# Kernel optimization log

Measured on AMD Instinct MI355X. Metric: run time of the kernel, lower is better.

## Reference

```python
import jax, jax.numpy as jnp
import numpy as np

EMBED_DIM = 1280
NUM_HEADS = 20
HEAD_DIM = EMBED_DIM // NUM_HEADS
SEQ = 1024
BSZ = 8
ROPE_BASE = 10000.0


def _rope_cos_sin(seq_len, dim, dtype):
    # ESM RotaryEmbedding: inv_freq over even indices, emb = concat(freqs, freqs)
    inv_freq = 1.0 / (ROPE_BASE ** (jnp.arange(0, dim, 2, dtype=jnp.float32) / dim))
    t = jnp.arange(seq_len, dtype=jnp.float32)
    freqs = t[:, None] * inv_freq[None, :]          # [S, D/2]
    emb = jnp.concatenate([freqs, freqs], axis=-1)  # [S, D]
    return jnp.cos(emb).astype(dtype), jnp.sin(emb).astype(dtype)


def _rotate_half(x):
    x1, x2 = jnp.split(x, 2, axis=-1)
    return jnp.concatenate([-x2, x1], axis=-1)


def _apply_rotary(x, cos, sin):
    # x: [B, H, S, D]; cos/sin: [S, D] broadcast over B, H
    return x * cos[None, None, :, :] + _rotate_half(x) * sin[None, None, :, :]


def setup_inputs() -> dict:
    key = jax.random.key(0)
    ks = jax.random.split(key, 9)
    s = 0.02
    return {
        "query": jax.random.normal(ks[0], (SEQ, BSZ, EMBED_DIM), jnp.float32),
        "q_w": jax.random.normal(ks[1], (EMBED_DIM, EMBED_DIM), jnp.float32) * s,
        "q_b": jax.random.normal(ks[2], (EMBED_DIM,), jnp.float32) * s,
        "k_w": jax.random.normal(ks[3], (EMBED_DIM, EMBED_DIM), jnp.float32) * s,
        "k_b": jax.random.normal(ks[4], (EMBED_DIM,), jnp.float32) * s,
        "v_w": jax.random.normal(ks[5], (EMBED_DIM, EMBED_DIM), jnp.float32) * s,
        "v_b": jax.random.normal(ks[6], (EMBED_DIM,), jnp.float32) * s,
        "out_w": jax.random.normal(ks[7], (EMBED_DIM, EMBED_DIM), jnp.float32) * s,
        "out_b": jax.random.normal(ks[8], (EMBED_DIM,), jnp.float32) * s,
    }


def reference(query, q_w, q_b, k_w, k_b, v_w, v_b, out_w, out_b):
    T, B, E = query.shape
    H, D = NUM_HEADS, HEAD_DIM
    scaling = D ** -0.5

    # Separate Q/K/V projections (self-attention: key = value = query)
    q = query @ q_w.T + q_b
    k = query @ k_w.T + k_b
    v = query @ v_w.T + v_b

    # [T, B, E] -> [B, H, T, D]
    def split_heads(x):
        return x.reshape(T, B, H, D).transpose(1, 2, 0, 3)

    q, k, v = split_heads(q), split_heads(k), split_heads(v)

    # Rotary embeddings on q, k
    cos, sin = _rope_cos_sin(T, D, q.dtype)
    q = _apply_rotary(q, cos, sin)
    k = _apply_rotary(k, cos, sin)

    # SDPA with explicit scale = head_dim^-0.5
    scores = jnp.einsum("bhtd,bhsd->bhts", q, k) * scaling
    probs = jax.nn.softmax(scores, axis=-1)
    attn = jnp.einsum("bhts,bhsd->bhtd", probs, v)  # [B, H, T, D]

    # [B, H, T, D] -> [T, B, E]
    attn = attn.transpose(2, 0, 1, 3).reshape(T, B, E)
    return attn @ out_w.T + out_b
```

## Files before the change

### kernel.cpp

```cpp
#include <hip/hip_runtime.h>
#include <math.h>

#define T_SEQ 1024
#define BSZ   8
#define EMB   1280
#define NH    20
#define HD    64
#define MROWS 8192
#define KBYTES (EMB * 2)

typedef __attribute__((ext_vector_type(8))) short bf16x8;
typedef __attribute__((ext_vector_type(4))) float f32x4;

__device__ __forceinline__ short f2bf(float f) {
    unsigned u = __float_as_uint(f);
    u += 0x7fff + ((u >> 16) & 1);
    return (short)(u >> 16);
}
__device__ __forceinline__ float bf2f(short s) {
    return __uint_as_float(((unsigned)(unsigned short)s) << 16);
}

__device__ __forceinline__ void gld16(const void* g, void* l) {
    __builtin_amdgcn_global_load_lds(
        (const __attribute__((address_space(1))) void*)g,
        (__attribute__((address_space(3))) void*)l, 16, 0, 0);
}

__global__ __launch_bounds__(256) void f2bf_kernel(
    const float* __restrict__ in, short* __restrict__ out, int n8)
{
    int i = blockIdx.x * 256 + threadIdx.x;
    if (i >= n8) return;
    const float4* p = (const float4*)in;
    float4 x = p[2 * i], y = p[2 * i + 1];
    bf16x8 o;
    o[0] = f2bf(x.x); o[1] = f2bf(x.y); o[2] = f2bf(x.z); o[3] = f2bf(x.w);
    o[4] = f2bf(y.x); o[5] = f2bf(y.y); o[6] = f2bf(y.z); o[7] = f2bf(y.w);
    ((bf16x8*)out)[i] = o;
}

__global__ __launch_bounds__(256) void wcast_kernel(
    const float* __restrict__ w0, const float* __restrict__ w1,
    const float* __restrict__ w2, const float* __restrict__ w3,
    short* __restrict__ o0, short* __restrict__ o1,
    short* __restrict__ o2, short* __restrict__ o3, int n8)
{
    int which = blockIdx.y;
    const float* in = (which == 0) ? w0 : (which == 1) ? w1 : (which == 2) ? w2 : w3;
    short* out      = (which == 0) ? o0 : (which == 1) ? o1 : (which == 2) ? o2 : o3;
    int i = blockIdx.x * 256 + threadIdx.x;
    if (i >= n8) return;
    const float4* p = (const float4*)in;
    float4 x = p[2 * i], y = p[2 * i + 1];
    bf16x8 o;
    o[0] = f2bf(x.x); o[1] = f2bf(x.y); o[2] = f2bf(x.z); o[3] = f2bf(x.w);
    o[4] = f2bf(y.x); o[5] = f2bf(y.y); o[6] = f2bf(y.z); o[7] = f2bf(y.w);
    ((bf16x8*)out)[i] = o;
}

__global__ void rope_table_kernel(float* __restrict__ cost, float* __restrict__ sint) {
    int idx = blockIdx.x * 256 + threadIdx.x;
    if (idx >= T_SEQ * 32) return;
    int i = idx & 31, t = idx >> 5;
    float inv = powf(10000.0f, -(float)i / 32.0f);
    float f = (float)t * inv;
    cost[idx] = cosf(f);
    sint[idx] = sinf(f);
}

__device__ __forceinline__ void gemm_core(
    const short* __restrict__ A, const short* __restrict__ B,
    char* As, char* Bs, int m0, int n0, int tid, f32x4 (&acc)[4][4])
{
    const int l   = tid & 63;
    const int wid = tid >> 6;
    const int wr  = wid >> 1, wc = wid & 1;

    const int srow = l >> 3;
    const int scol = ((l & 7) ^ srow) << 4;
    const int g16  = (l >> 4) << 4;
    const int swx  = (l & 7) << 4;

    for (int k0 = 0; k0 < EMB; k0 += 64) {
        __syncthreads();
        #pragma unroll
        for (int c = 0; c < 4; ++c) {
            int ch  = wid * 4 + c;
            int row = ch * 8 + srow;
            gld16((const char*)A + (size_t)(m0 + row) * KBYTES + k0 * 2 + scol,
                  As + ch * 1024);
            gld16((const char*)B + (size_t)(n0 + row) * KBYTES + k0 * 2 + scol,
                  Bs + ch * 1024);
        }
        __syncthreads();
        #pragma unroll
        for (int kk = 0; kk < 2; ++kk) {
            const int cb = (kk * 64 + g16) ^ swx;
            bf16x8 af[4], bfr[4];
            #pragma unroll
            for (int m = 0; m < 4; ++m)
                af[m] = *(const bf16x8*)(As + (wr * 64 + m * 16 + (l & 15)) * 128 + cb);
            #pragma unroll
            for (int n = 0; n < 4; ++n)
                bfr[n] = *(const bf16x8*)(Bs + (wc * 64 + n * 16 + (l & 15)) * 128 + cb);
            #pragma unroll
            for (int m = 0; m < 4; ++m)
                #pragma unroll
                for (int n = 0; n < 4; ++n)
                    acc[m][n] = __builtin_amdgcn_mfma_f32_16x16x32_bf16(
                        af[m], bfr[n], acc[m][n], 0, 0, 0);
        }
    }
}

__global__ __launch_bounds__(256) void qkv_gemm_kernel(
    const short* __restrict__ A,
    const short* __restrict__ B0, const short* __restrict__ B1, const short* __restrict__ B2,
    const float* __restrict__ bias0, const float* __restrict__ bias1, const float* __restrict__ bias2,
    const float* __restrict__ cost, const float* __restrict__ sint,
    short* __restrict__ O0, short* __restrict__ O1, short* __restrict__ O2)
{
    __shared__ short As_s[8192];
    __shared__ short Bs_s[8192];

    const int z = blockIdx.z;
    const short* B = (z == 0) ? B0 : (z == 1) ? B1 : B2;
    const float* bias = (z == 0) ? bias0 : (z == 1) ? bias1 : bias2;
    short* O = (z == 0) ? O0 : (z == 1) ? O1 : O2;
    const float scale = (z == 0) ? 0.125f : 1.0f;

    const int tid = threadIdx.x;
    const int l = tid & 63;
    const int wid = tid >> 6;
    const int wr = wid >> 1, wc = wid & 1;
    const int m0 = blockIdx.x * 128;
    const int n0 = blockIdx.y * 128;

    f32x4 acc[4][4];
    const f32x4 z4 = {0.f, 0.f, 0.f, 0.f};
    #pragma unroll
    for (int m = 0; m < 4; ++m)
        #pragma unroll
        for (int n = 0; n < 4; ++n) acc[m][n] = z4;

    gemm_core(A, B, (char*)As_s, (char*)Bs_s, m0, n0, tid, acc);

    #pragma unroll
    for (int n = 0; n < 4; ++n) {
        int col = n0 + wc * 64 + n * 16 + (l & 15);
        float bv = bias[col];
        #pragma unroll
        for (int m = 0; m < 4; ++m)
            #pragma unroll
            for (int r = 0; r < 4; ++r) acc[m][n][r] += bv;
    }

    if (z < 2) {
        #pragma unroll
        for (int m = 0; m < 4; ++m) {
            #pragma unroll
            for (int r = 0; r < 4; ++r) {
                int row = m0 + wr * 64 + m * 16 + (l >> 4) * 4 + r;
                int t = row >> 3;
                #pragma unroll
                for (int n = 0; n < 2; ++n) {
                    int i = n * 16 + (l & 15);
                    float c = cost[t * 32 + i];
                    float s = sint[t * 32 + i];
                    float x1 = acc[m][n][r], x2 = acc[m][n + 2][r];
                    acc[m][n][r]     = x1 * c - x2 * s;
                    acc[m][n + 2][r] = x2 * c + x1 * s;
                }
            }
        }
    }

    #pragma unroll
    for (int n = 0; n < 4; ++n) {
        int col = n0 + wc * 64 + n * 16 + (l & 15);
        int h = col >> 6, d = col & 63;
        #pragma unroll
        for (int m = 0; m < 4; ++m) {
            #pragma unroll
            for (int r = 0; r < 4; ++r) {
                int row = m0 + wr * 64 + m * 16 + (l >> 4) * 4 + r;
                int t = row >> 3, b = row & 7;
                O[((size_t)(b * NH + h) * T_SEQ + t) * HD + d] = f2bf(acc[m][n][r] * scale);
            }
        }
    }
}

__global__ __launch_bounds__(256) void out_gemm_kernel(
    const short* __restrict__ A, const short* __restrict__ B,
    const float* __restrict__ bias, float* __restrict__ O)
{
    __shared__ short As_s[8192];
    __shared__ short Bs_s[8192];

    const int tid = threadIdx.x;
    const int l = tid & 63;
    const int wid = tid >> 6;
    const int wr = wid >> 1, wc = wid & 1;
    const int m0 = blockIdx.x * 128;
    const int n0 = blockIdx.y * 128;

    f32x4 acc[4][4];
    const f32x4 z4 = {0.f, 0.f, 0.f, 0.f};
    #pragma unroll
    for (int m = 0; m < 4; ++m)
        #pragma unroll
        for (int n = 0; n < 4; ++n) acc[m][n] = z4;

    gemm_core(A, B, (char*)As_s, (char*)Bs_s, m0, n0, tid, acc);

    #pragma unroll
    for (int n = 0; n < 4; ++n) {
        int col = n0 + wc * 64 + n * 16 + (l & 15);
        float bv = bias[col];
        #pragma unroll
        for (int m = 0; m < 4; ++m) {
            #pragma unroll
            for (int r = 0; r < 4; ++r) {
                int row = m0 + wr * 64 + m * 16 + (l >> 4) * 4 + r;
                O[(size_t)row * EMB + col] = acc[m][n][r] + bv;
            }
        }
    }
}

__global__ __launch_bounds__(256) void transpose_v_kernel(
    const short* __restrict__ v, short* __restrict__ vt)
{
    __shared__ short tv[64][72];
    const int tid = threadIdx.x;
    const int bh = blockIdx.y, t0 = blockIdx.x * 64;
    const short* src = v + ((size_t)bh * T_SEQ + t0) * HD;
    #pragma unroll
    for (int p = 0; p < 2; ++p) {
        int row = p * 32 + (tid >> 3);
        int c8 = (tid & 7) * 8;
        *(bf16x8*)&tv[row][c8] = *(const bf16x8*)(src + row * HD + c8);
    }
    __syncthreads();
    short* dst = vt + (size_t)bh * (HD * T_SEQ) + t0;
    #pragma unroll
    for (int p = 0; p < 2; ++p) {
        int d = p * 32 + (tid >> 3);
        int t8 = (tid & 7) * 8;
        bf16x8 o;
        #pragma unroll
        for (int j = 0; j < 8; ++j) o[j] = tv[t8 + j][d];
        *(bf16x8*)(dst + (size_t)d * T_SEQ + t8) = o;
    }
}

__global__ __launch_bounds__(256) void attn_kernel(
    const short* __restrict__ Q, const short* __restrict__ K,
    const short* __restrict__ Vt, short* __restrict__ Aout)
{
    __shared__ short Ks_s[8192];
    __shared__ short Vs_s[8192];
    __shared__ short Ps_s[4096];
    char* Ks = (char*)Ks_s;
    char* Vs = (char*)Vs_s;
    char* Ps = (char*)Ps_s;

    const int tid = threadIdx.x;
    const int l = tid & 63;
    const int w = tid >> 6;
    const int g = l >> 4;

    const int bid = blockIdx.y * 16 + blockIdx.x;
    const int swz = (bid & 7) * 320 + (bid >> 3);
    const int q0 = (swz & 15) * 64;
    const int bh = swz >> 4;

    const int srow = l >> 3;
    const int scol = ((l & 7) ^ srow) << 4;
    const int g16  = g << 4;
    const int swx  = (l & 7) << 4;

    const short* Qg = Q + (size_t)bh * (T_SEQ * HD);
    const short* Kg = K + (size_t)bh * (T_SEQ * HD);
    const short* Vg = Vt + (size_t)bh * (HD * T_SEQ);

    #pragma unroll
    for (int c = 0; c < 2; ++c) {
        int ch = w * 2 + c;
        int row = ch * 8 + srow;
        gld16((const char*)Qg + (size_t)(q0 + row) * HD * 2 + scol, Ps + ch * 1024);
        gld16((const char*)Kg + (size_t)(row) * HD * 2 + scol, Ks + ch * 1024);
        gld16((const char*)Vg + ((size_t)row * T_SEQ) * 2 + scol, Vs + ch * 1024);
    }
    __syncthreads();

    bf16x8 qf[2];
    #pragma unroll
    for (int kk = 0; kk < 2; ++kk)
        qf[kk] = *(const bf16x8*)(Ps + (w * 16 + (l & 15)) * 128 + ((kk * 64 + g16) ^ swx));

    f32x4 oacc[4];
    const f32x4 z4 = {0.f, 0.f, 0.f, 0.f};
    #pragma unroll
    for (int n = 0; n < 4; ++n) oacc[n] = z4;
    float m_i = -INFINITY;
    float l_i = 0.f;

    const int pbase = (w * 16 + (l & 15)) * 128;

    int buf = 0;
    for (int kt = 0; kt < T_SEQ / 64; ++kt) {
        if (kt + 1 < T_SEQ / 64) {
            const int ob = (buf ^ 1) * 8192;
            #pragma unroll
            for (int c = 0; c < 2; ++c) {
                int ch = w * 2 + c;
                int row = ch * 8 + srow;
                gld16((const char*)Kg + (size_t)((kt + 1) * 64 + row) * HD * 2 + scol,
                      Ks + ob + ch * 1024);
                gld16((const char*)Vg + ((size_t)row * T_SEQ + (kt + 1) * 64) * 2 + scol,
                      Vs + ob + ch * 1024);
            }
        }
        const int cbuf = buf * 8192;

        f32x4 sT[4];
        #pragma unroll
        for (int n = 0; n < 4; ++n) sT[n] = z4;
        __builtin_amdgcn_s_setprio(1);
        #pragma unroll
        for (int kk = 0; kk < 2; ++kk) {
            const int cb = (kk * 64 + g16) ^ swx;
            #pragma unroll
            for (int n = 0; n < 4; ++n) {
                bf16x8 kf = *(const bf16x8*)(Ks + cbuf + (n * 16 + (l & 15)) * 128 + cb);
                sT[n] = __builtin_amdgcn_mfma_f32_16x16x32_bf16(kf, qf[kk], sT[n], 0, 0, 0);
            }
        }
        __builtin_amdgcn_s_setprio(0);

        float pmax = fmaxf(fmaxf(sT[0][0], sT[0][1]), fmaxf(sT[0][2], sT[0][3]));
        #pragma unroll
        for (int n = 1; n < 4; ++n)
            pmax = fmaxf(pmax, fmaxf(fmaxf(sT[n][0], sT[n][1]), fmaxf(sT[n][2], sT[n][3])));
        pmax = fmaxf(pmax, __shfl_xor(pmax, 16));
        pmax = fmaxf(pmax, __shfl_xor(pmax, 32));

        if (__any(pmax > m_i + 8.0f)) {
            float mn = fmaxf(m_i, pmax);
            float corr = __expf(m_i - mn);
            m_i = mn;
            l_i *= corr;
            #pragma unroll
            for (int r = 0; r < 4; ++r) {
                float cp = __shfl(corr, (l & 48) | (g * 4 + r));
                #pragma unroll
                for (int n = 0; n < 4; ++n) oacc[n][r] *= cp;
            }
        }

        float lsum = 0.f;
        #pragma unroll
        for (int n = 0; n < 4; ++n) {
            float p0 = __expf(sT[n][0] - m_i);
            float p1 = __expf(sT[n][1] - m_i);
            float p2 = __expf(sT[n][2] - m_i);
            float p3 = __expf(sT[n][3] - m_i);
            lsum += (p0 + p1) + (p2 + p3);
            unsigned lo = ((unsigned)(unsigned short)f2bf(p0)) |
                          (((unsigned)(unsigned short)f2bf(p1)) << 16);
            unsigned hi = ((unsigned)(unsigned short)f2bf(p2)) |
                          (((unsigned)(unsigned short)f2bf(p3)) << 16);
            uint2 pk; pk.x = lo; pk.y = hi;
            *(uint2*)(Ps + pbase + ((n * 32 + g * 8) ^ swx)) = pk;
        }
        lsum += __shfl_xor(lsum, 16);
        lsum += __shfl_xor(lsum, 32);
        l_i += lsum;

        __builtin_amdgcn_s_setprio(1);
        #pragma unroll
        for (int kk = 0; kk < 2; ++kk) {
            const int cb = (kk * 64 + g16) ^ swx;
            bf16x8 ap = *(const bf16x8*)(Ps + pbase + cb);
            #pragma unroll
            for (int n = 0; n < 4; ++n) {
                bf16x8 bv = *(const bf16x8*)(Vs + cbuf + (n * 16 + (l & 15)) * 128 + cb);
                oacc[n] = __builtin_amdgcn_mfma_f32_16x16x32_bf16(ap, bv, oacc[n], 0, 0, 0);
            }
        }
        __builtin_amdgcn_s_setprio(0);

        __syncthreads();
        buf ^= 1;
    }

    float inv = 1.0f / l_i;
    float invp[4];
    #pragma unroll
    for (int r = 0; r < 4; ++r) invp[r] = __shfl(inv, (l & 48) | (g * 4 + r));

    const int b_ = bh / NH, h = bh % NH;
    #pragma unroll
    for (int n = 0; n < 4; ++n) {
        int d = h * HD + n * 16 + (l & 15);
        #pragma unroll
        for (int r = 0; r < 4; ++r) {
            int t = q0 + w * 16 + g * 4 + r;
            Aout[((size_t)t * BSZ + b_) * EMB + d] = f2bf(oacc[n][r] * invp[r]);
        }
    }
}

extern "C" void kernel_launch(void* const* d_in, const int* in_sizes, int n_in,
                              void* d_out, int out_size, void* d_ws, size_t ws_size,
                              hipStream_t stream) {
    const float* X     = (const float*)d_in[0];
    const float* q_w   = (const float*)d_in[1];
    const float* q_b   = (const float*)d_in[2];
    const float* k_w   = (const float*)d_in[3];
    const float* k_b   = (const float*)d_in[4];
    const float* v_w   = (const float*)d_in[5];
    const float* v_b   = (const float*)d_in[6];
    const float* out_w = (const float*)d_in[7];
    const float* out_b = (const float*)d_in[8];
    float* out = (float*)d_out;

    short* ws = (short*)d_ws;
    const size_t NACT = (size_t)MROWS * EMB;
    const size_t NW   = (size_t)EMB * EMB;
    short* xb  = ws;
    short* wqb = xb + NACT;
    short* wkb = wqb + NW;
    short* wvb = wkb + NW;
    short* wob = wvb + NW;
    short* qb  = wob + NW;
    short* kb  = qb + NACT;
    short* vb  = kb + NACT;
    short* vtb = vb + NACT;
    short* ab  = vtb + NACT;
    float* cost = (float*)(ab + NACT);
    float* sint = cost + T_SEQ * 32;

    rope_table_kernel<<<dim3(128), 256, 0, stream>>>(cost, sint);
    f2bf_kernel<<<dim3(5120), 256, 0, stream>>>(X, xb, (int)(NACT / 8));
    wcast_kernel<<<dim3(800, 4), 256, 0, stream>>>(
        q_w, k_w, v_w, out_w, wqb, wkb, wvb, wob, (int)(NW / 8));

    qkv_gemm_kernel<<<dim3(MROWS / 128, EMB / 128, 3), 256, 0, stream>>>(
        xb, wqb, wkb, wvb, q_b, k_b, v_b, cost, sint, qb, kb, vb);

    transpose_v_kernel<<<dim3(T_SEQ / 64, BSZ * NH), 256, 0, stream>>>(vb, vtb);

    attn_kernel<<<dim3(T_SEQ / 64, BSZ * NH), 256, 0, stream>>>(qb, kb, vtb, ab);

    out_gemm_kernel<<<dim3(MROWS / 128, EMB / 128), 256, 0, stream>>>(
        ab, wob, out_b, out);
}
```

Measured before the change: 377.6 us.

## Double-buffer LDS with 512-thread 256x128 GEMM tiles and async prefetch

Rewrites the shared GEMM core to use two LDS buffers, prefetching k-tile t+2 with global_load_lds while computing tile t, using explicit vmcnt waits and barriers. Block size grows to 512 threads (8 waves) covering a 256x128 output tile, and setprio raises MFMA priority. The aim is to hide global-load latency and halve B-tile reloads per output row. In exchange, LDS use rises to 96KB per block, which lowers occupancy, and the grid for each GEMM gets smaller.

```diff
diff --git a/kernel.cpp b/kernel.cpp
--- a/kernel.cpp
+++ b/kernel.cpp
@@ -8,6 +8,7 @@
 #define HD    64
 #define MROWS 8192
 #define KBYTES (EMB * 2)
+#define NKT   20
 
 typedef __attribute__((ext_vector_type(8))) short bf16x8;
 typedef __attribute__((ext_vector_type(4))) float f32x4;
@@ -69,31 +70,50 @@
     sint[idx] = sinf(f);
 }
 
-__device__ __forceinline__ void gemm_core(
+__device__ __forceinline__ void gemm_stage(
     const short* __restrict__ A, const short* __restrict__ B,
-    char* As, char* Bs, int m0, int n0, int tid, f32x4 (&acc)[4][4])
+    char* As, char* Bs, int m0, int n0, int k0, int w, int srow, int scol)
+{
+    #pragma unroll
+    for (int c = 0; c < 4; ++c) {
+        int ch = w * 4 + c;
+        int row = ch * 8 + srow;
+        gld16((const char*)A + (size_t)(m0 + row) * KBYTES + k0 * 2 + scol,
+              As + ch * 1024);
+    }
+    #pragma unroll
+    for (int c = 0; c < 2; ++c) {
+        int ch = w * 2 + c;
+        int row = ch * 8 + srow;
+        gld16((const char*)B + (size_t)(n0 + row) * KBYTES + k0 * 2 + scol,
+              Bs + ch * 1024);
+    }
+}
+
+__device__ __forceinline__ void gemm_core512(
+    const short* __restrict__ A, const short* __restrict__ B,
+    char* As0, char* Bs0, char* As1, char* Bs1,
+    int m0, int n0, int tid, f32x4 (&acc)[4][4])
 {
     const int l   = tid & 63;
-    const int wid = tid >> 6;
-    const int wr  = wid >> 1, wc = wid & 1;
+    const int w   = tid >> 6;
+    const int wr  = w >> 1, wc = w & 1;
 
     const int srow = l >> 3;
     const int scol = ((l & 7) ^ srow) << 4;
     const int g16  = (l >> 4) << 4;
     const int swx  = (l & 7) << 4;
 
-    for (int k0 = 0; k0 < EMB; k0 += 64) {
-        __syncthreads();
-        #pragma unroll
-        for (int c = 0; c < 4; ++c) {
-            int ch  = wid * 4 + c;
-            int row = ch * 8 + srow;
-            gld16((const char*)A + (size_t)(m0 + row) * KBYTES + k0 * 2 + scol,
-                  As + ch * 1024);
-            gld16((const char*)B + (size_t)(n0 + row) * KBYTES + k0 * 2 + scol,
-                  Bs + ch * 1024);
-        }
-        __syncthreads();
+    gemm_stage(A, B, As0, Bs0, m0, n0, 0,  w, srow, scol);
+    gemm_stage(A, B, As1, Bs1, m0, n0, 64, w, srow, scol);
+    asm volatile("s_waitcnt vmcnt(6)" ::: "memory");
+    __builtin_amdgcn_s_barrier();
+    asm volatile("" ::: "memory");
+
+    for (int t = 0; t < NKT; ++t) {
+        char* As = (t & 1) ? As1 : As0;
+        char* Bs = (t & 1) ? Bs1 : Bs0;
+
         #pragma unroll
         for (int kk = 0; kk < 2; ++kk) {
             const int cb = (kk * 64 + g16) ^ swx;
@@ -104,25 +124,41 @@
             #pragma unroll
             for (int n = 0; n < 4; ++n)
                 bfr[n] = *(const bf16x8*)(Bs + (wc * 64 + n * 16 + (l & 15)) * 128 + cb);
+            __builtin_amdgcn_s_setprio(1);
             #pragma unroll
             for (int m = 0; m < 4; ++m)
                 #pragma unroll
                 for (int n = 0; n < 4; ++n)
                     acc[m][n] = __builtin_amdgcn_mfma_f32_16x16x32_bf16(
                         af[m], bfr[n], acc[m][n], 0, 0, 0);
-        }
-    }
-}
-
-__global__ __launch_bounds__(256) void qkv_gemm_kernel(
+            __builtin_amdgcn_s_setprio(0);
+        }
+
+        asm volatile("" ::: "memory");
+        __builtin_amdgcn_s_barrier();
+        asm volatile("" ::: "memory");
+
+        if (t + 2 < NKT)
+            gemm_stage(A, B, As, Bs, m0, n0, (t + 2) * 64, w, srow, scol);
+
+        if (t + 2 < NKT) { asm volatile("s_waitcnt vmcnt(6)" ::: "memory"); }
+        else             { asm volatile("s_waitcnt vmcnt(0)" ::: "memory"); }
+        __builtin_amdgcn_s_barrier();
+        asm volatile("" ::: "memory");
+    }
+}
+
+__global__ __launch_bounds__(512) void qkv_gemm_kernel(
     const short* __restrict__ A,
     const short* __restrict__ B0, const short* __restrict__ B1, const short* __restrict__ B2,
     const float* __restrict__ bias0, const float* __restrict__ bias1, const float* __restrict__ bias2,
     const float* __restrict__ cost, const float* __restrict__ sint,
     short* __restrict__ O0, short* __restrict__ O1, short* __restrict__ O2)
 {
-    __shared__ short As_s[8192];
-    __shared__ short Bs_s[8192];
+    __shared__ short As0_s[16384];
+    __shared__ short Bs0_s[8192];
+    __shared__ short As1_s[16384];
+    __shared__ short Bs1_s[8192];
 
     const int z = blockIdx.z;
     const short* B = (z == 0) ? B0 : (z == 1) ? B1 : B2;
@@ -134,7 +170,7 @@
     const int l = tid & 63;
     const int wid = tid >> 6;
     const int wr = wid >> 1, wc = wid & 1;
-    const int m0 = blockIdx.x * 128;
+    const int m0 = blockIdx.x * 256;
     const int n0 = blockIdx.y * 128;
 
     f32x4 acc[4][4];
@@ -144,7 +180,8 @@
         #pragma unroll
         for (int n = 0; n < 4; ++n) acc[m][n] = z4;
 
-    gemm_core(A, B, (char*)As_s, (char*)Bs_s, m0, n0, tid, acc);
+    gemm_core512(A, B, (char*)As0_s, (char*)Bs0_s, (char*)As1_s, (char*)Bs1_s,
+                 m0, n0, tid, acc);
 
     #pragma unroll
     for (int n = 0; n < 4; ++n) {
@@ -192,18 +229,20 @@
     }
 }
 
-__global__ __launch_bounds__(256) void out_gemm_kernel(
+__global__ __launch_bounds__(512) void out_gemm_kernel(
     const short* __restrict__ A, const short* __restrict__ B,
     const float* __restrict__ bias, float* __restrict__ O)
 {
-    __shared__ short As_s[8192];
-    __shared__ short Bs_s[8192];
+    __shared__ short As0_s[16384];
+    __shared__ short Bs0_s[8192];
+    __shared__ short As1_s[16384];
+    __shared__ short Bs1_s[8192];
 
     const int tid = threadIdx.x;
     const int l = tid & 63;
     const int wid = tid >> 6;
     const int wr = wid >> 1, wc = wid & 1;
-    const int m0 = blockIdx.x * 128;
+    const int m0 = blockIdx.x * 256;
     const int n0 = blockIdx.y * 128;
 
     f32x4 acc[4][4];
@@ -213,7 +252,8 @@
         #pragma unroll
         for (int n = 0; n < 4; ++n) acc[m][n] = z4;
 
-    gemm_core(A, B, (char*)As_s, (char*)Bs_s, m0, n0, tid, acc);
+    gemm_core512(A, B, (char*)As0_s, (char*)Bs0_s, (char*)As1_s, (char*)Bs1_s,
+                 m0, n0, tid, acc);
 
     #pragma unroll
     for (int n = 0; n < 4; ++n) {
@@ -449,13 +489,13 @@
     wcast_kernel<<<dim3(800, 4), 256, 0, stream>>>(
         q_w, k_w, v_w, out_w, wqb, wkb, wvb, wob, (int)(NW / 8));
 
-    qkv_gemm_kernel<<<dim3(MROWS / 128, EMB / 128, 3), 256, 0, stream>>>(
+    qkv_gemm_kernel<<<dim3(MROWS / 256, EMB / 128, 3), 512, 0, stream>>>(
         xb, wqb, wkb, wvb, q_b, k_b, v_b, cost, sint, qb, kb, vb);
 
     transpose_v_kernel<<<dim3(T_SEQ / 64, BSZ * NH), 256, 0, stream>>>(vb, vtb);
 
     attn_kernel<<<dim3(T_SEQ / 64, BSZ * NH), 256, 0, stream>>>(qb, kb, vtb, ab);
 
-    out_gemm_kernel<<<dim3(MROWS / 128, EMB / 128), 256, 0, stream>>>(
+    out_gemm_kernel<<<dim3(MROWS / 256, EMB / 128), 512, 0, stream>>>(
         ab, wob, out_b, out);
 }
```

Result: slower. 403.9 us (+7.0%).
